# Kernel tuning notes

Hardware: AMD Instinct MI355X
Metric: run time of the kernel (lower is better)

Reference implementation:

```python
import jax, jax.numpy as jnp
import numpy as np

ETA = 0.1      # self.eta
BETA = 0.05    # self.beta
MU = 0.05      # self.mu
MINI = 1e-6    # mini_val
SEEDS_PER_TOPIC = 10


def setup_inputs() -> dict:
    key = jax.random.key(0)
    k1, k2, k3, k4 = jax.random.split(key, 4)
    B, V, K = 64, 10000, 64
    # sparse-ish bag-of-words counts in {0,1,2}
    batch_BOW = jax.random.randint(k1, (B, V), 0, 3).astype(jnp.float32)
    # disjoint seed words: SEEDS_PER_TOPIC seed words per topic
    seeds = jnp.zeros((V, K), jnp.float32)
    rows = jnp.arange(SEEDS_PER_TOPIC * K)
    cols = jnp.repeat(jnp.arange(K), SEEDS_PER_TOPIC)
    seeds = seeds.at[rows, cols].set(1.0)
    exp_m = jax.random.uniform(k2, (B, K), jnp.float32) * 10.0     # E[m_dk] for docs in batch
    exp_s = jax.random.uniform(k3, (V, K), jnp.float32) * 5.0 * seeds  # E[s_wk], nonzero only at seed entries
    exp_n = jax.random.uniform(k4, (V, K), jnp.float32) * 5.0      # E[n_wk]
    pi = jnp.full((K,), 0.7, jnp.float32)
    return {"batch_BOW": batch_BOW, "seeds": seeds, "exp_m": exp_m,
            "exp_s": exp_s, "exp_n": exp_n, "pi": pi}


def reference(batch_BOW, seeds, exp_m, exp_s, exp_n, pi):
    # Vectorized SCVB0_guided over the whole minibatch (no per-doc Python loop).
    V, K = seeds.shape
    S = seeds.sum(0)                      # [K] number of seed words per topic
    beta_sum = BETA * V                   # self.beta_sum[guided_m]
    mu_sum = MU * S                       # [K]
    exp_s_sum = exp_s.sum(0)              # [K]
    exp_n_sum = exp_n.sum(0)              # [K]

    mask = (batch_BOW > 0).astype(batch_BOW.dtype)[:, :, None]   # [B,V,1] BOW_nonzero gather
    theta = exp_m[:, None, :] + ETA                               # [B,1,K]
    phi_s = (MU + exp_s) / (mu_sum + exp_s_sum)                   # [V,K]
    phi_n = (BETA + exp_n) / (beta_sum + exp_n_sum)               # [V,K]

    g_ss = mask * seeds[None] * theta * phi_s[None] * pi          # [B,V,K]
    g_sr = mask * seeds[None] * theta * phi_n[None] * (1.0 - pi)
    g_rr = mask * (1.0 - seeds[None]) * theta * phi_n[None]

    s_sum = g_ss.sum(-1, keepdims=True) + g_sr.sum(-1, keepdims=True)
    r_sum = g_rr.sum(-1, keepdims=True)
    g_ss = g_ss / (s_sum + MINI)
    g_sr = g_sr / (s_sum + MINI)
    g_rr = g_rr / (r_sum + MINI)

    # seed word <=> word is seed of at least one topic; else use g_rr only
    is_seed = (seeds.sum(1) > 0)[None, :, None]                   # [1,V,1]
    gamma = jnp.where(is_seed, pi * g_ss + (1.0 - pi) * (g_sr + g_rr), g_rr)

    counts = batch_BOW[:, :, None]                                # [B,V,1]
    temp_exp_m_batch = (gamma * counts).sum(1)                    # [B,K]
    temp_exp_n = ((g_sr + g_rr) * counts).sum(0)                  # [V,K] scatter-accumulate
    temp_exp_s = (g_ss * counts).sum(0)                           # [V,K]
    gamma_sr_sum = g_sr.sum((0, 1))                               # [K]
    exp_q_z = (gamma * jnp.log(gamma + MINI)).sum()               # scalar entropy term
    return temp_exp_m_batch, temp_exp_n, temp_exp_s, gamma_sr_sum, exp_q_z
```

## Files before the change

kernel.cpp:

```cpp
#include <hip/hip_runtime.h>
#include <hip/hip_bf16.h>

#define ETA_C  0.1f
#define BETA_C 0.05f
#define MU_C   0.05f
#define MINI_C 1e-6f

typedef __attribute__((ext_vector_type(8))) short short8;
typedef __attribute__((ext_vector_type(4))) float f32x4;

template<int CTRL, int ROWMASK>
__device__ __forceinline__ float dpp_add(float x) {
  int v = __builtin_amdgcn_update_dpp(0, __float_as_int(x), CTRL, ROWMASK, 0xf, true);
  return x + __int_as_float(v);
}

__device__ __forceinline__ float wave_sum(float x) {
  x = dpp_add<0xB1,  0xF>(x);
  x = dpp_add<0x4E,  0xF>(x);
  x = dpp_add<0x141, 0xF>(x);
  x = dpp_add<0x140, 0xF>(x);
  x = dpp_add<0x142, 0xA>(x);
  x = dpp_add<0x143, 0xC>(x);
  return __int_as_float(__builtin_amdgcn_readlane(__float_as_int(x), 63));
}

__device__ __forceinline__ float rl(float x, int k) {
  return __int_as_float(__builtin_amdgcn_readlane(__float_as_int(x), k));
}

__device__ __forceinline__ short bf16r(float x) {
  unsigned u = __float_as_uint(x);
  u += 0x7fffu + ((u >> 16) & 1u);
  return (short)(u >> 16);
}

__global__ __launch_bounds__(256) void sums_kernel(
    const float* __restrict__ seeds, const float* __restrict__ es,
    const float* __restrict__ en, float* __restrict__ part,
    float* __restrict__ out, int V, int rows_per_block, int gsr_off,
    int zeroOut) {
  __shared__ float sh[192];
  int t = threadIdx.x, bx = blockIdx.x;
  if (zeroOut) {
    if (bx < 16) out[(bx << 8) + t] = 0.f;
    else if (bx == 16 && t < 65) out[gsr_off + t] = 0.f;
  }
  if (t < 192) sh[t] = 0.f;
  __syncthreads();
  int k = t & 63, w = t >> 6;
  int v0 = bx * rows_per_block;
  int v1 = min(v0 + rows_per_block, V);
  float s0 = 0.f, s1 = 0.f, s2 = 0.f;
  for (int v = v0 + w; v < v1; v += 4) {
    int idx = (v << 6) + k;
    s0 += seeds[idx]; s1 += es[idx]; s2 += en[idx];
  }
  atomicAdd(&sh[k], s0);
  atomicAdd(&sh[64 + k], s1);
  atomicAdd(&sh[128 + k], s2);
  __syncthreads();
  if (t < 192) part[bx * 192 + t] = sh[t];
}

__global__ __launch_bounds__(1024, 4) void main_kernel(
    const float* __restrict__ bow,
    const float* __restrict__ seeds,
    const float* __restrict__ exp_m,
    const float* __restrict__ exp_s,
    const float* __restrict__ exp_n,
    const float* __restrict__ pi,
    const float* __restrict__ part,
    float* __restrict__ out,
    float* __restrict__ wsm, float* __restrict__ wsgq,
    int V, int useWs, int gsr_off) {
  __shared__ float thF[4096];
  __shared__ short THbf[4096];
  __shared__ short THTbf[4096];
  __shared__ short TLbf[4096];
  __shared__ short ARRT[1024];
  __shared__ short ASVT[1024];
  __shared__ short ARLT[1024];
  __shared__ short WSRT[2048];
  __shared__ short PKA[2048];
  __shared__ short CIRT[1024];
  __shared__ float RSL[64 * 17];
  __shared__ float SSL[64 * 17];
  __shared__ float L0a[64 * 17];
  __shared__ float L0b[64 * 17];
  __shared__ float sums_sh[192];
  float* NNL = RSL;
  float* red_gsr = SSL;
  float* redq = L0a;

  int t = threadIdx.x;
#pragma unroll
  for (int i = 0; i < 4; i++) {
    int idx = t + (i << 10);
    int b = idx >> 6, k = idx & 63;
    float th = exp_m[idx] + ETA_C;
    float lth = __logf(th);
    thF[idx] = th;
    THbf[idx] = bf16r(th);
    THTbf[(k << 6) + b] = bf16r(th);
    TLbf[idx] = bf16r(th * lth);
  }
  if (t < 192) {
    float s = 0.f;
#pragma unroll 8
    for (int j = 0; j < 64; j++) s += part[j * 192 + t];
    sums_sh[t] = s;
  }
  __syncthreads();

  int lane = t & 63, w = t >> 6;
  int v = (blockIdx.x << 4) + w;
  bool active = (v < V);
  int q = lane >> 4, c = lane & 15;

  float pik = 0.f, omp = 0.f, a_ss = 0.f, a_sr = 0.f, a_rr = 0.f;
  float bowpre = 0.f;
  bool seedRow = false;
  if (active) {
    int rbase = (v << 6) + lane;
    float seed = seeds[rbase];
    float es = exp_s[rbase];
    float en = exp_n[rbase];
    pik = pi[lane];
    float inv_ds = __builtin_amdgcn_rcpf(MU_C * sums_sh[lane] + sums_sh[64 + lane]);
    float inv_dn = __builtin_amdgcn_rcpf(BETA_C * (float)V + sums_sh[128 + lane]);
    float phi_s = (MU_C + es) * inv_ds;
    float phi_n = (BETA_C + en) * inv_dn;
    omp = 1.0f - pik;
    a_ss = seed * phi_s * pik;
    a_sr = seed * phi_n * omp;
    a_rr = (1.0f - seed) * phi_n;
    seedRow = (__ballot(seed > 0.f) != 0ull);
    float wsv = fmaf(pik, a_ss, omp * a_sr);
    float wrv = seedRow ? omp * a_rr : a_rr;
    float arrl = (a_rr > 0.f) ? a_rr * __logf(a_rr) : 0.f;
    ARRT[(w << 6) + lane] = bf16r(a_rr);
    ASVT[(w << 6) + lane] = bf16r(a_ss + a_sr);
    ARLT[(w << 6) + lane] = bf16r(arrl);
    WSRT[(lane << 5) + w] = bf16r(wsv);
    WSRT[(lane << 5) + 16 + w] = bf16r(wrv);
    bowpre = bow[lane * V + v];
  } else {
    ARRT[(w << 6) + lane] = 0;
    ASVT[(w << 6) + lane] = 0;
    ARLT[(w << 6) + lane] = 0;
    WSRT[(lane << 5) + w] = 0;
    WSRT[(lane << 5) + 16 + w] = 0;
  }
  __syncthreads();

  {
    int job = w >> 2, mt = w & 3;
    const short* Amat = (job == 3) ? TLbf : THbf;
    const short* Bmat = (job == 0) ? ARRT : (job == 1) ? ASVT
                       : (job == 2) ? ARLT : ARRT;
    float* Cd = (job == 0) ? RSL : (job == 1) ? SSL : (job == 2) ? L0a : L0b;
    f32x4 acc = {0.f, 0.f, 0.f, 0.f};
    int arow = (mt << 4) + c;
#pragma unroll
    for (int s = 0; s < 2; s++) {
      short8 af = *(const short8*)&Amat[(arow << 6) + (s << 5) + (q << 3)];
      short8 bf = *(const short8*)&Bmat[(c << 6) + (s << 5) + (q << 3)];
      acc = __builtin_amdgcn_mfma_f32_16x16x32_bf16(af, bf, acc, 0, 0, 0);
    }
#pragma unroll
    for (int r = 0; r < 4; r++)
      Cd[((mt << 4) + (q << 2) + r) * 17 + c] = acc[r];
  }
  __syncthreads();

  float acc_s = 0.f, acc_g = 0.f, acc_qk = 0.f, acc_qb = 0.f;
  if (active) {
    float rsv = RSL[lane * 17 + w];
    float ssv = SSL[lane * 17 + w];
    float ivx = __builtin_amdgcn_rcpf(ssv + MINI_C);
    float ivy = __builtin_amdgcn_rcpf(rsv + MINI_C);
    float cis = bowpre * ivx;
    float cirr = bowpre * ivy;
    PKA[(lane << 5) + w] = bf16r(cis);
    PKA[(lane << 5) + 16 + w] = bf16r(cirr);
    CIRT[(w << 6) + lane] = bf16r(cirr);
    if (!seedRow) {
      float Lb = L0a[lane * 17 + w] + L0b[lane * 17 + w];
      float q0 = (bowpre > 0.f) ? ivy : 0.f;
      float q1 = q0 * __logf(ivy);
      acc_qb = fmaf(q0, Lb, q1 * rsv);
      out[4096 + V * 64 + (v << 6) + lane] = 0.f;
    } else {
      float acc_n = 0.f;
      unsigned long long m = __ballot(bowpre > 0.f);
      while (m) {
        int b = __builtin_amdgcn_readfirstlane(__builtin_ctzll(m));
        m &= (m - 1);
        float cb = rl(bowpre, b);
        float is = rl(ivx, b), ir = rl(ivy, b);
        float th = thF[(b << 6) + lane];
        float gss = th * a_ss * is;
        float gsr = th * a_sr * is;
        float grr = th * a_rr * ir;
        float gnr = gsr + grr;
        float gamma = fmaf(pik, gss, omp * gnr);
        acc_n = fmaf(gnr, cb, acc_n);
        acc_s = fmaf(gss, cb, acc_s);
        acc_g += gsr;
        acc_qk = fmaf(gamma, __logf(gamma + MINI_C), acc_qk);
      }
      out[4096 + (v << 6) + lane] = acc_n;
      out[4096 + V * 64 + (v << 6) + lane] = acc_s;
    }
  } else {
    PKA[(lane << 5) + w] = 0;
    PKA[(lane << 5) + 16 + w] = 0;
    CIRT[(w << 6) + lane] = 0;
  }
  __syncthreads();

  {
    int tm = w >> 2, tn = w & 3;
    f32x4 acc = {0.f, 0.f, 0.f, 0.f};
    short8 af = *(const short8*)&PKA[(((tm << 4) + c) << 5) + (q << 3)];
    short8 bf = *(const short8*)&WSRT[(((tn << 4) + c) << 5) + (q << 3)];
    acc = __builtin_amdgcn_mfma_f32_16x16x32_bf16(af, bf, acc, 0, 0, 0);
#pragma unroll
    for (int r = 0; r < 4; r++) {
      int brow = (tm << 4) + (q << 2) + r;
      int kcol = (tn << 4) + c;
      float val = acc[r] * thF[(brow << 6) + kcol];
      if (useWs) wsm[blockIdx.x * 4096 + (brow << 6) + kcol] = val;
      else atomicAdd(&out[(brow << 6) + kcol], val);
    }
    if (w >= 12) {
      int mt = w - 12;
      f32x4 an = {0.f, 0.f, 0.f, 0.f};
#pragma unroll
      for (int s = 0; s < 2; s++) {
        short8 a2 = *(const short8*)&THTbf[(((mt << 4) + c) << 6) + (s << 5) + (q << 3)];
        short8 b2 = *(const short8*)&CIRT[(c << 6) + (s << 5) + (q << 3)];
        an = __builtin_amdgcn_mfma_f32_16x16x32_bf16(a2, b2, an, 0, 0, 0);
      }
#pragma unroll
      for (int r = 0; r < 4; r++)
        NNL[((mt << 4) + (q << 2) + r) * 17 + c] = an[r];
    }
  }
  __syncthreads();

  if (active && !seedRow)
    out[4096 + (v << 6) + lane] = a_rr * NNL[lane * 17 + w];

  red_gsr[t] = acc_g;
  float qzw = wave_sum(acc_qk + acc_qb);
  if (lane == 0) redq[w] = qzw;
  __syncthreads();

  if (w == 0) {
    float g = 0.f;
#pragma unroll
    for (int j = 0; j < 16; j++) g += red_gsr[(j << 6) + lane];
    if (useWs) wsgq[blockIdx.x * 66 + lane] = g;
    else if (g != 0.f) atomicAdd(&out[gsr_off + lane], g);
    if (t == 0) {
      float qs = 0.f;
#pragma unroll
      for (int j = 0; j < 16; j++) qs += redq[j];
      if (useWs) wsgq[blockIdx.x * 66 + 64] = qs;
      else atomicAdd(&out[gsr_off + 64], qs);
    }
  }
}

__global__ __launch_bounds__(1024) void reduce_kernel(
    const float* __restrict__ wsm, const float* __restrict__ wsgq,
    float* __restrict__ out, int NB, int gsr_off) {
  __shared__ float sh[1024];
  int t = threadIdx.x, lane = t & 63, w = t >> 6, bx = blockIdx.x;
  if (bx < 64) {
    int e = (bx << 6) + lane;
    float s0 = 0.f, s1 = 0.f, s2 = 0.f, s3 = 0.f;
    int j = w;
    for (; j + 48 < NB; j += 64) {
      s0 += wsm[(size_t)(j)      * 4096 + e];
      s1 += wsm[(size_t)(j + 16) * 4096 + e];
      s2 += wsm[(size_t)(j + 32) * 4096 + e];
      s3 += wsm[(size_t)(j + 48) * 4096 + e];
    }
    for (; j < NB; j += 16) s0 += wsm[(size_t)j * 4096 + e];
    sh[t] = (s0 + s1) + (s2 + s3);
    __syncthreads();
    if (w == 0) {
      float tot = 0.f;
#pragma unroll
      for (int i = 0; i < 16; i++) tot += sh[(i << 6) + lane];
      out[e] = tot;
    }
  } else if (bx == 64) {
    float s = 0.f;
    for (int j = w; j < NB; j += 16) s += wsgq[j * 66 + lane];
    sh[t] = s;
    __syncthreads();
    if (w == 0) {
      float tot = 0.f;
#pragma unroll
      for (int i = 0; i < 16; i++) tot += sh[(i << 6) + lane];
      out[gsr_off + lane] = tot;
    }
  } else {
    float s = 0.f;
    for (int j = t; j < NB; j += 1024) s += wsgq[j * 66 + 64];
    s = wave_sum(s);
    if (lane == 0) sh[w] = s;
    __syncthreads();
    if (t == 0) {
      float tot = 0.f;
#pragma unroll
      for (int i = 0; i < 16; i++) tot += sh[i];
      out[gsr_off + 64] = tot;
    }
  }
}

extern "C" void kernel_launch(void* const* d_in, const int* in_sizes, int n_in,
                              void* d_out, int out_size, void* d_ws,
                              size_t ws_size, hipStream_t stream) {
  (void)n_in; (void)out_size;
  const float* bow   = (const float*)d_in[0];
  const float* seeds = (const float*)d_in[1];
  const float* exp_m = (const float*)d_in[2];
  const float* exp_s = (const float*)d_in[3];
  const float* exp_n = (const float*)d_in[4];
  const float* pi    = (const float*)d_in[5];
  int K = in_sizes[5];
  int V = in_sizes[1] / K;
  float* out = (float*)d_out;
  float* ws = (float*)d_ws;

  int NB = (V + 15) / 16;
  int gsr_off = 4096 + 2 * V * 64;

  size_t needF = (size_t)NB * 4096 + (size_t)NB * 66 + 64 * 192;
  int useWs = (ws_size >= needF * 4) ? 1 : 0;

  float* wsm  = ws;
  float* wsgq = wsm + (size_t)NB * 4096;
  float* part = wsgq + (size_t)NB * 66;

  int rpb = (V + 63) / 64;
  sums_kernel<<<64, 256, 0, stream>>>(seeds, exp_s, exp_n, part, out, V, rpb,
                                      gsr_off, useWs ? 0 : 1);
  main_kernel<<<NB, 1024, 0, stream>>>(bow, seeds, exp_m, exp_s, exp_n, pi,
                                       part, out, wsm, wsgq, V, useWs, gsr_off);
  if (useWs) {
    reduce_kernel<<<66, 1024, 0, stream>>>(wsm, wsgq, out, NB, gsr_off);
  }
}
```

Before: 117.4 us.

## Make main kernel persistent over vocab tiles to amortize theta setup

The main kernel now launches at most 512 blocks, and each block loops over several 16-word vocab tiles. The per-block theta tables and the seed-sum reduction are built once per block and reused across tiles, where before every one of the 625 blocks rebuilt them. The fp32 theta table is dropped, and theta is rebuilt from the bf16 copy, which cuts shared memory but adds bf16 rounding to the seed-row gamma path. The gsr and entropy partials are accumulated across tiles, so the reduce kernel reads only NP partial rows.

```diff
diff --git a/kernel.cpp b/kernel.cpp
--- a/kernel.cpp
+++ b/kernel.cpp
@@ -33,6 +33,10 @@
   unsigned u = __float_as_uint(x);
   u += 0x7fffu + ((u >> 16) & 1u);
   return (short)(u >> 16);
+}
+
+__device__ __forceinline__ float bf2f(short s) {
+  return __uint_as_float(((unsigned)(unsigned short)s) << 16);
 }
 
 __global__ __launch_bounds__(256) void sums_kernel(
@@ -73,8 +77,7 @@
     const float* __restrict__ part,
     float* __restrict__ out,
     float* __restrict__ wsm, float* __restrict__ wsgq,
-    int V, int useWs, int gsr_off) {
-  __shared__ float thF[4096];
+    int V, int useWs, int gsr_off, int NB) {
   __shared__ short THbf[4096];
   __shared__ short THTbf[4096];
   __shared__ short TLbf[4096];
@@ -100,7 +103,6 @@
     int b = idx >> 6, k = idx & 63;
     float th = exp_m[idx] + ETA_C;
     float lth = __logf(th);
-    thF[idx] = th;
     THbf[idx] = bf16r(th);
     THTbf[(k << 6) + b] = bf16r(th);
     TLbf[idx] = bf16r(th * lth);
@@ -114,147 +116,154 @@
   __syncthreads();
 
   int lane = t & 63, w = t >> 6;
-  int v = (blockIdx.x << 4) + w;
-  bool active = (v < V);
   int q = lane >> 4, c = lane & 15;
-
-  float pik = 0.f, omp = 0.f, a_ss = 0.f, a_sr = 0.f, a_rr = 0.f;
-  float bowpre = 0.f;
-  bool seedRow = false;
-  if (active) {
-    int rbase = (v << 6) + lane;
-    float seed = seeds[rbase];
-    float es = exp_s[rbase];
-    float en = exp_n[rbase];
-    pik = pi[lane];
-    float inv_ds = __builtin_amdgcn_rcpf(MU_C * sums_sh[lane] + sums_sh[64 + lane]);
-    float inv_dn = __builtin_amdgcn_rcpf(BETA_C * (float)V + sums_sh[128 + lane]);
-    float phi_s = (MU_C + es) * inv_ds;
-    float phi_n = (BETA_C + en) * inv_dn;
-    omp = 1.0f - pik;
-    a_ss = seed * phi_s * pik;
-    a_sr = seed * phi_n * omp;
-    a_rr = (1.0f - seed) * phi_n;
-    seedRow = (__ballot(seed > 0.f) != 0ull);
-    float wsv = fmaf(pik, a_ss, omp * a_sr);
-    float wrv = seedRow ? omp * a_rr : a_rr;
-    float arrl = (a_rr > 0.f) ? a_rr * __logf(a_rr) : 0.f;
-    ARRT[(w << 6) + lane] = bf16r(a_rr);
-    ASVT[(w << 6) + lane] = bf16r(a_ss + a_sr);
-    ARLT[(w << 6) + lane] = bf16r(arrl);
-    WSRT[(lane << 5) + w] = bf16r(wsv);
-    WSRT[(lane << 5) + 16 + w] = bf16r(wrv);
-    bowpre = bow[lane * V + v];
-  } else {
-    ARRT[(w << 6) + lane] = 0;
-    ASVT[(w << 6) + lane] = 0;
-    ARLT[(w << 6) + lane] = 0;
-    WSRT[(lane << 5) + w] = 0;
-    WSRT[(lane << 5) + 16 + w] = 0;
-  }
-  __syncthreads();
-
-  {
-    int job = w >> 2, mt = w & 3;
-    const short* Amat = (job == 3) ? TLbf : THbf;
-    const short* Bmat = (job == 0) ? ARRT : (job == 1) ? ASVT
-                       : (job == 2) ? ARLT : ARRT;
-    float* Cd = (job == 0) ? RSL : (job == 1) ? SSL : (job == 2) ? L0a : L0b;
-    f32x4 acc = {0.f, 0.f, 0.f, 0.f};
-    int arow = (mt << 4) + c;
-#pragma unroll
-    for (int s = 0; s < 2; s++) {
-      short8 af = *(const short8*)&Amat[(arow << 6) + (s << 5) + (q << 3)];
-      short8 bf = *(const short8*)&Bmat[(c << 6) + (s << 5) + (q << 3)];
+  float acc_g_tot = 0.f, acc_q_tot = 0.f;
+
+  for (int tile = blockIdx.x; tile < NB; tile += gridDim.x) {
+    int v = (tile << 4) + w;
+    bool active = (v < V);
+
+    float pik = 0.f, omp = 0.f, a_ss = 0.f, a_sr = 0.f, a_rr = 0.f;
+    float bowpre = 0.f;
+    bool seedRow = false;
+    if (active) {
+      int rbase = (v << 6) + lane;
+      float seed = seeds[rbase];
+      float es = exp_s[rbase];
+      float en = exp_n[rbase];
+      pik = pi[lane];
+      float inv_ds = __builtin_amdgcn_rcpf(MU_C * sums_sh[lane] + sums_sh[64 + lane]);
+      float inv_dn = __builtin_amdgcn_rcpf(BETA_C * (float)V + sums_sh[128 + lane]);
+      float phi_s = (MU_C + es) * inv_ds;
+      float phi_n = (BETA_C + en) * inv_dn;
+      omp = 1.0f - pik;
+      a_ss = seed * phi_s * pik;
+      a_sr = seed * phi_n * omp;
+      a_rr = (1.0f - seed) * phi_n;
+      seedRow = (__ballot(seed > 0.f) != 0ull);
+      float wsv = fmaf(pik, a_ss, omp * a_sr);
+      float wrv = seedRow ? omp * a_rr : a_rr;
+      float arrl = (a_rr > 0.f) ? a_rr * __logf(a_rr) : 0.f;
+      ARRT[(w << 6) + lane] = bf16r(a_rr);
+      ASVT[(w << 6) + lane] = bf16r(a_ss + a_sr);
+      ARLT[(w << 6) + lane] = bf16r(arrl);
+      WSRT[(lane << 5) + w] = bf16r(wsv);
+      WSRT[(lane << 5) + 16 + w] = bf16r(wrv);
+      bowpre = bow[lane * V + v];
+    } else {
+      ARRT[(w << 6) + lane] = 0;
+      ASVT[(w << 6) + lane] = 0;
+      ARLT[(w << 6) + lane] = 0;
+      WSRT[(lane << 5) + w] = 0;
+      WSRT[(lane << 5) + 16 + w] = 0;
+    }
+    __syncthreads();
+
+    {
+      int job = w >> 2, mt = w & 3;
+      const short* Amat = (job == 3) ? TLbf : THbf;
+      const short* Bmat = (job == 0) ? ARRT : (job == 1) ? ASVT
+                         : (job == 2) ? ARLT : ARRT;
+      float* Cd = (job == 0) ? RSL : (job == 1) ? SSL : (job == 2) ? L0a : L0b;
+      f32x4 acc = {0.f, 0.f, 0.f, 0.f};
+      int arow = (mt << 4) + c;
+#pragma unroll
+      for (int s = 0; s < 2; s++) {
+        short8 af = *(const short8*)&Amat[(arow << 6) + (s << 5) + (q << 3)];
+        short8 bf = *(const short8*)&Bmat[(c << 6) + (s << 5) + (q << 3)];
+        acc = __builtin_amdgcn_mfma_f32_16x16x32_bf16(af, bf, acc, 0, 0, 0);
+      }
+#pragma unroll
+      for (int r = 0; r < 4; r++)
+        Cd[((mt << 4) + (q << 2) + r) * 17 + c] = acc[r];
+    }
+    __syncthreads();
+
+    float acc_s = 0.f, acc_g = 0.f, acc_qk = 0.f, acc_qb = 0.f;
+    if (active) {
+      float rsv = RSL[lane * 17 + w];
+      float ssv = SSL[lane * 17 + w];
+      float ivx = __builtin_amdgcn_rcpf(ssv + MINI_C);
+      float ivy = __builtin_amdgcn_rcpf(rsv + MINI_C);
+      float cis = bowpre * ivx;
+      float cirr = bowpre * ivy;
+      PKA[(lane << 5) + w] = bf16r(cis);
+      PKA[(lane << 5) + 16 + w] = bf16r(cirr);
+      CIRT[(w << 6) + lane] = bf16r(cirr);
+      if (!seedRow) {
+        float Lb = L0a[lane * 17 + w] + L0b[lane * 17 + w];
+        float q0 = (bowpre > 0.f) ? ivy : 0.f;
+        float q1 = q0 * __logf(ivy);
+        acc_qb = fmaf(q0, Lb, q1 * rsv);
+        out[4096 + V * 64 + (v << 6) + lane] = 0.f;
+      } else {
+        float acc_n = 0.f;
+        unsigned long long m = __ballot(bowpre > 0.f);
+        while (m) {
+          int b = __builtin_amdgcn_readfirstlane(__builtin_ctzll(m));
+          m &= (m - 1);
+          float cb = rl(bowpre, b);
+          float is = rl(ivx, b), ir = rl(ivy, b);
+          float th = bf2f(THbf[(b << 6) + lane]);
+          float gss = th * a_ss * is;
+          float gsr = th * a_sr * is;
+          float grr = th * a_rr * ir;
+          float gnr = gsr + grr;
+          float gamma = fmaf(pik, gss, omp * gnr);
+          acc_n = fmaf(gnr, cb, acc_n);
+          acc_s = fmaf(gss, cb, acc_s);
+          acc_g += gsr;
+          acc_qk = fmaf(gamma, __logf(gamma + MINI_C), acc_qk);
+        }
+        out[4096 + (v << 6) + lane] = acc_n;
+        out[4096 + V * 64 + (v << 6) + lane] = acc_s;
+      }
+    } else {
+      PKA[(lane << 5) + w] = 0;
+      PKA[(lane << 5) + 16 + w] = 0;
+      CIRT[(w << 6) + lane] = 0;
+    }
+    acc_g_tot += acc_g;
+    acc_q_tot += acc_qk + acc_qb;
+    __syncthreads();
+
+    {
+      int tm = w >> 2, tn = w & 3;
+      f32x4 acc = {0.f, 0.f, 0.f, 0.f};
+      short8 af = *(const short8*)&PKA[(((tm << 4) + c) << 5) + (q << 3)];
+      short8 bf = *(const short8*)&WSRT[(((tn << 4) + c) << 5) + (q << 3)];
       acc = __builtin_amdgcn_mfma_f32_16x16x32_bf16(af, bf, acc, 0, 0, 0);
-    }
-#pragma unroll
-    for (int r = 0; r < 4; r++)
-      Cd[((mt << 4) + (q << 2) + r) * 17 + c] = acc[r];
-  }
-  __syncthreads();
-
-  float acc_s = 0.f, acc_g = 0.f, acc_qk = 0.f, acc_qb = 0.f;
-  if (active) {
-    float rsv = RSL[lane * 17 + w];
-    float ssv = SSL[lane * 17 + w];
-    float ivx = __builtin_amdgcn_rcpf(ssv + MINI_C);
-    float ivy = __builtin_amdgcn_rcpf(rsv + MINI_C);
-    float cis = bowpre * ivx;
-    float cirr = bowpre * ivy;
-    PKA[(lane << 5) + w] = bf16r(cis);
-    PKA[(lane << 5) + 16 + w] = bf16r(cirr);
-    CIRT[(w << 6) + lane] = bf16r(cirr);
-    if (!seedRow) {
-      float Lb = L0a[lane * 17 + w] + L0b[lane * 17 + w];
-      float q0 = (bowpre > 0.f) ? ivy : 0.f;
-      float q1 = q0 * __logf(ivy);
-      acc_qb = fmaf(q0, Lb, q1 * rsv);
-      out[4096 + V * 64 + (v << 6) + lane] = 0.f;
-    } else {
-      float acc_n = 0.f;
-      unsigned long long m = __ballot(bowpre > 0.f);
-      while (m) {
-        int b = __builtin_amdgcn_readfirstlane(__builtin_ctzll(m));
-        m &= (m - 1);
-        float cb = rl(bowpre, b);
-        float is = rl(ivx, b), ir = rl(ivy, b);
-        float th = thF[(b << 6) + lane];
-        float gss = th * a_ss * is;
-        float gsr = th * a_sr * is;
-        float grr = th * a_rr * ir;
-        float gnr = gsr + grr;
-        float gamma = fmaf(pik, gss, omp * gnr);
-        acc_n = fmaf(gnr, cb, acc_n);
-        acc_s = fmaf(gss, cb, acc_s);
-        acc_g += gsr;
-        acc_qk = fmaf(gamma, __logf(gamma + MINI_C), acc_qk);
+#pragma unroll
+      for (int r = 0; r < 4; r++) {
+        int brow = (tm << 4) + (q << 2) + r;
+        int kcol = (tn << 4) + c;
+        float val = acc[r] * bf2f(THbf[(brow << 6) + kcol]);
+        if (useWs) wsm[(size_t)tile * 4096 + (brow << 6) + kcol] = val;
+        else atomicAdd(&out[(brow << 6) + kcol], val);
       }
-      out[4096 + (v << 6) + lane] = acc_n;
-      out[4096 + V * 64 + (v << 6) + lane] = acc_s;
-    }
-  } else {
-    PKA[(lane << 5) + w] = 0;
-    PKA[(lane << 5) + 16 + w] = 0;
-    CIRT[(w << 6) + lane] = 0;
-  }
-  __syncthreads();
-
-  {
-    int tm = w >> 2, tn = w & 3;
-    f32x4 acc = {0.f, 0.f, 0.f, 0.f};
-    short8 af = *(const short8*)&PKA[(((tm << 4) + c) << 5) + (q << 3)];
-    short8 bf = *(const short8*)&WSRT[(((tn << 4) + c) << 5) + (q << 3)];
-    acc = __builtin_amdgcn_mfma_f32_16x16x32_bf16(af, bf, acc, 0, 0, 0);
-#pragma unroll
-    for (int r = 0; r < 4; r++) {
-      int brow = (tm << 4) + (q << 2) + r;
-      int kcol = (tn << 4) + c;
-      float val = acc[r] * thF[(brow << 6) + kcol];
-      if (useWs) wsm[blockIdx.x * 4096 + (brow << 6) + kcol] = val;
-      else atomicAdd(&out[(brow << 6) + kcol], val);
-    }
-    if (w >= 12) {
-      int mt = w - 12;
-      f32x4 an = {0.f, 0.f, 0.f, 0.f};
-#pragma unroll
-      for (int s = 0; s < 2; s++) {
-        short8 a2 = *(const short8*)&THTbf[(((mt << 4) + c) << 6) + (s << 5) + (q << 3)];
-        short8 b2 = *(const short8*)&CIRT[(c << 6) + (s << 5) + (q << 3)];
-        an = __builtin_amdgcn_mfma_f32_16x16x32_bf16(a2, b2, an, 0, 0, 0);
+      if (w >= 12) {
+        int mt = w - 12;
+        f32x4 an = {0.f, 0.f, 0.f, 0.f};
+#pragma unroll
+        for (int s = 0; s < 2; s++) {
+          short8 a2 = *(const short8*)&THTbf[(((mt << 4) + c) << 6) + (s << 5) + (q << 3)];
+          short8 b2 = *(const short8*)&CIRT[(c << 6) + (s << 5) + (q << 3)];
+          an = __builtin_amdgcn_mfma_f32_16x16x32_bf16(a2, b2, an, 0, 0, 0);
+        }
+#pragma unroll
+        for (int r = 0; r < 4; r++)
+          NNL[((mt << 4) + (q << 2) + r) * 17 + c] = an[r];
       }
-#pragma unroll
-      for (int r = 0; r < 4; r++)
-        NNL[((mt << 4) + (q << 2) + r) * 17 + c] = an[r];
-    }
-  }
-  __syncthreads();
-
-  if (active && !seedRow)
-    out[4096 + (v << 6) + lane] = a_rr * NNL[lane * 17 + w];
-
-  red_gsr[t] = acc_g;
-  float qzw = wave_sum(acc_qk + acc_qb);
+    }
+    __syncthreads();
+
+    if (active && !seedRow)
+      out[4096 + (v << 6) + lane] = a_rr * NNL[lane * 17 + w];
+  }
+
+  __syncthreads();
+  red_gsr[t] = acc_g_tot;
+  float qzw = wave_sum(acc_q_tot);
   if (lane == 0) redq[w] = qzw;
   __syncthreads();
 
@@ -276,7 +285,7 @@
 
 __global__ __launch_bounds__(1024) void reduce_kernel(
     const float* __restrict__ wsm, const float* __restrict__ wsgq,
-    float* __restrict__ out, int NB, int gsr_off) {
+    float* __restrict__ out, int NB, int NP, int gsr_off) {
   __shared__ float sh[1024];
   int t = threadIdx.x, lane = t & 63, w = t >> 6, bx = blockIdx.x;
   if (bx < 64) {
@@ -300,7 +309,7 @@
     }
   } else if (bx == 64) {
     float s = 0.f;
-    for (int j = w; j < NB; j += 16) s += wsgq[j * 66 + lane];
+    for (int j = w; j < NP; j += 16) s += wsgq[j * 66 + lane];
     sh[t] = s;
     __syncthreads();
     if (w == 0) {
@@ -311,7 +320,7 @@
     }
   } else {
     float s = 0.f;
-    for (int j = t; j < NB; j += 1024) s += wsgq[j * 66 + 64];
+    for (int j = t; j < NP; j += 1024) s += wsgq[j * 66 + 64];
     s = wave_sum(s);
     if (lane == 0) sh[w] = s;
     __syncthreads();
@@ -340,6 +349,7 @@
   float* ws = (float*)d_ws;
 
   int NB = (V + 15) / 16;
+  int NP = NB < 512 ? NB : 512;
   int gsr_off = 4096 + 2 * V * 64;
 
   size_t needF = (size_t)NB * 4096 + (size_t)NB * 66 + 64 * 192;
@@ -352,9 +362,10 @@
   int rpb = (V + 63) / 64;
   sums_kernel<<<64, 256, 0, stream>>>(seeds, exp_s, exp_n, part, out, V, rpb,
                                       gsr_off, useWs ? 0 : 1);
-  main_kernel<<<NB, 1024, 0, stream>>>(bow, seeds, exp_m, exp_s, exp_n, pi,
-                                       part, out, wsm, wsgq, V, useWs, gsr_off);
+  main_kernel<<<NP, 1024, 0, stream>>>(bow, seeds, exp_m, exp_s, exp_n, pi,
+                                       part, out, wsm, wsgq, V, useWs, gsr_off,
+                                       NB);
   if (useWs) {
-    reduce_kernel<<<66, 1024, 0, stream>>>(wsm, wsgq, out, NB, gsr_off);
-  }
-}
+    reduce_kernel<<<66, 1024, 0, stream>>>(wsm, wsgq, out, NB, NP, gsr_off);
+  }
+}
```

New measurement: 119.0 us. Within noise of the previous version (+1.3%).
